# Optimization experiments

Hardware: AMD Instinct MI355X
Metric: run time of the kernel (lower is better)

## Reference

```python
import jax, jax.numpy as jnp
import numpy as np

B, T, D, H = 2, 2048, 1024, 16
DK = D // H


def setup_inputs() -> dict:
    key = jax.random.key(0)
    ks = jax.random.split(key, 11)
    s = 1.0 / np.sqrt(D)
    return {
        "x_q": jax.random.normal(ks[0], (B, T, D), jnp.float32),
        "x_kv": jax.random.normal(ks[1], (B, T, D), jnp.float32),
        "mask": jnp.ones((B, 1, T, T), jnp.int32),
        "Wq": jax.random.normal(ks[2], (D, D), jnp.float32) * s,
        "bq": jnp.zeros((D,), jnp.float32),
        "Wk": jax.random.normal(ks[3], (D, D), jnp.float32) * s,
        "bk": jnp.zeros((D,), jnp.float32),
        "Wv": jax.random.normal(ks[4], (D, D), jnp.float32) * s,
        "bv": jnp.zeros((D,), jnp.float32),
        "Wo": jax.random.normal(ks[5], (D, D), jnp.float32) * s,
        "bo": jnp.zeros((D,), jnp.float32),
    }


def _split_heads(x):
    # (B, T, D) -> (B, H, T, DK)
    b, t, _ = x.shape
    return x.reshape(b, t, H, DK).transpose(0, 2, 1, 3)


def reference(x_q, x_kv, mask, Wq, bq, Wk, bk, Wv, bv, Wo, bo):
    # Linear layers use torch convention: y = x @ W.T + b
    Q = _split_heads(x_q @ Wq.T + bq)   # (B,H,Tq,DK)
    K = _split_heads(x_kv @ Wk.T + bk)  # (B,H,Tk,DK)
    V = _split_heads(x_kv @ Wv.T + bv)  # (B,H,Tk,DK)

    scores = jnp.einsum("bhqd,bhkd->bhqk", Q, K) / jnp.sqrt(jnp.float32(DK))
    scores = jnp.where(mask == 0, jnp.float32(-jnp.inf), scores)
    attn = jax.nn.softmax(scores, axis=-1)  # (B,H,Tq,Tk)

    out = jnp.einsum("bhqk,bhkd->bhqd", attn, V)
    out = out.transpose(0, 2, 1, 3).reshape(B, T, D)  # combine heads
    out = out @ Wo.T + bo
    return out, attn
```

## Files before the change

kernel.cpp:

```cpp
#include <hip/hip_runtime.h>
#include <hip/hip_bf16.h>

#define DEVINL __device__ __forceinline__

typedef __attribute__((ext_vector_type(4))) float f32x4;
typedef __attribute__((ext_vector_type(8))) short short8;
typedef __attribute__((ext_vector_type(4))) short short4v;

constexpr int CB = 2, CT = 2048, CD = 1024, CH = 16, CDK = 64;
constexpr int CM = CB * CT;
constexpr float LOG2E = 1.44269504088896340736f;

DEVINL ushort f2bf(float f) {
  __hip_bfloat16 h = __float2bfloat16(f);
  ushort u; __builtin_memcpy(&u, &h, 2); return u;
}

DEVINL float bf2f(ushort u) {
  uint x = ((uint)u) << 16; float f; __builtin_memcpy(&f, &x, 4); return f;
}

DEVINL void gl2lds16(const ushort* g, ushort* ldsbase) {
  __builtin_amdgcn_global_load_lds(
      (const __attribute__((address_space(1))) void*)g,
      (__attribute__((address_space(3))) void*)ldsbase, 16, 0, 0);
}

__global__ void prep_kernel(const float* __restrict__ s0, ushort* __restrict__ d0, int n0,
                            const float* __restrict__ s1, ushort* __restrict__ d1, int n1,
                            const float* __restrict__ s2, ushort* __restrict__ d2, int n2,
                            const float* __restrict__ s3, ushort* __restrict__ d3, int n3,
                            const float* __restrict__ s4, ushort* __restrict__ d4, int n4,
                            const float* __restrict__ s5, ushort* __restrict__ d5, int n5,
                            const int* __restrict__ mask, uint* __restrict__ flags,
                            int cvt_blocks)
{
  if ((int)blockIdx.x >= cvt_blocks) {
    const int tile = blockIdx.x - cvt_blocks;
    const int b = tile >> 10, qb = (tile >> 5) & 31, kb = tile & 31;
    const int* base = mask + ((size_t)b * CT + qb * 64) * CT + kb * 64;
    const int r = threadIdx.x >> 2, c0 = (threadIdx.x & 3) * 16;
    int ok = 1;
    for (int j = 0; j < 4; ++j) {
      int4 v = *reinterpret_cast<const int4*>(base + (size_t)r * CT + c0 + j * 4);
      ok &= (v.x != 0) & (v.y != 0) & (v.z != 0) & (v.w != 0);
    }
    __shared__ int red[4];
    unsigned long long bal = __ballot(ok);
    if ((threadIdx.x & 63) == 0) red[threadIdx.x >> 6] = (bal == ~0ull);
    __syncthreads();
    if (threadIdx.x == 0) flags[tile] = (uint)(red[0] & red[1] & red[2] & red[3]);
    return;
  }
  int i = (blockIdx.x * blockDim.x + threadIdx.x) * 4;
  const float* s; ushort* d;
  if (i < n0) { s = s0; d = d0; }
  else if ((i -= n0) < n1) { s = s1; d = d1; }
  else if ((i -= n1) < n2) { s = s2; d = d2; }
  else if ((i -= n2) < n3) { s = s3; d = d3; }
  else if ((i -= n3) < n4) { s = s4; d = d4; }
  else if ((i -= n4) < n5) { s = s5; d = d5; }
  else return;
  float4 v = *reinterpret_cast<const float4*>(s + i);
  ushort4 o;
  o.x = f2bf(v.x); o.y = f2bf(v.y); o.z = f2bf(v.z); o.w = f2bf(v.w);
  *reinterpret_cast<ushort4*>(d + i) = o;
}

__global__ __launch_bounds__(256, 2)
void gemm_nt_kernel(const ushort* __restrict__ A, const ushort* __restrict__ Bm,
                    const float* __restrict__ bias1, const float* __restrict__ bias2,
                    void* __restrict__ Out, void* __restrict__ Out2,
                    int M, int N, int K, int mode, float scale)
{
  constexpr int BM = 128, BN = 64, BK = 32;
  __shared__ __align__(16) ushort As[2][BM * BK];
  __shared__ __align__(16) ushort Bs[2][BN * BK];
  const int tid = threadIdx.x;
  const int lane = tid & 63, wid = tid >> 6;
  const int wr = wid >> 1, wc = wid & 1;
  const int bm0 = blockIdx.y * BM, bn0 = blockIdx.x * BN;
  const int rsel = lane & 15, ksel = (lane >> 4) * 8;
  const int srow = lane >> 2, sc8 = (lane & 3) * 8;

  f32x4 acc[4][2];
  for (int i = 0; i < 4; ++i) for (int j = 0; j < 2; ++j) acc[i][j] = f32x4{0.f, 0.f, 0.f, 0.f};

  auto stage = [&](int bu, int k0) {
    const int ra0 = wid * 32;
    gl2lds16(&A[(size_t)(bm0 + ra0 + srow) * K + k0 + sc8],      &As[bu][ra0 * BK]);
    gl2lds16(&A[(size_t)(bm0 + ra0 + 16 + srow) * K + k0 + sc8], &As[bu][(ra0 + 16) * BK]);
    const int rb0 = wid * 16;
    gl2lds16(&Bm[(size_t)(bn0 + rb0 + srow) * K + k0 + sc8],     &Bs[bu][rb0 * BK]);
  };

  stage(0, 0);
  __syncthreads();
  const int NKT = K / BK;
  int bu = 0;
  for (int kt = 0; kt < NKT; ++kt) {
    if (kt + 1 < NKT) stage(bu ^ 1, (kt + 1) * BK);
    short8 af[4], bfr[2];
    for (int mi = 0; mi < 4; ++mi)
      af[mi] = *reinterpret_cast<short8*>(&As[bu][(wr * 64 + mi * 16 + rsel) * BK + ksel]);
    for (int ni = 0; ni < 2; ++ni)
      bfr[ni] = *reinterpret_cast<short8*>(&Bs[bu][(wc * 32 + ni * 16 + rsel) * BK + ksel]);
    for (int mi = 0; mi < 4; ++mi)
      for (int ni = 0; ni < 2; ++ni)
        acc[mi][ni] = __builtin_amdgcn_mfma_f32_16x16x32_bf16(af[mi], bfr[ni], acc[mi][ni], 0, 0, 0);
    if (kt + 1 < NKT) { __syncthreads(); bu ^= 1; }
  }

  const int r0 = (lane >> 4) * 4;
  for (int mi = 0; mi < 4; ++mi)
    for (int ni = 0; ni < 2; ++ni) {
      int gj = bn0 + wc * 32 + ni * 16 + rsel;
      float bv = (mode == 3 && gj >= 1024) ? bias2[gj - 1024] : bias1[gj];
      for (int r = 0; r < 4; ++r) {
        int gi = bm0 + wr * 64 + mi * 16 + r0 + r;
        float v = (acc[mi][ni][r] + bv) * scale;
        if (mode == 2) {
          reinterpret_cast<float*>(Out)[(size_t)gi * N + gj] = v;
        } else {
          int bb = gi >> 11, t = gi & (CT - 1);
          if (mode == 3 && gj >= 1024) {
            int gjv = gj - 1024;
            reinterpret_cast<ushort*>(Out2)[(((size_t)(bb * CH + (gjv >> 6)) * CDK + (gjv & 63)) * CT + t)] = f2bf(v);
          } else {
            reinterpret_cast<ushort*>(Out)[(((size_t)(bb * CH + (gj >> 6)) * CT + t) * CDK + (gj & 63))] = f2bf(v);
          }
        }
      }
    }
}

__global__ __launch_bounds__(512, 6)
void attn_kernel(const ushort* __restrict__ Qb, const ushort* __restrict__ Kb,
                 const ushort* __restrict__ Vt, const int* __restrict__ mask,
                 const uint* __restrict__ flags,
                 float* __restrict__ attn_out, ushort* __restrict__ oh)
{
  __shared__ __align__(16) ushort Ks[2][64 * 64];
  __shared__ __align__(16) ushort Vs[2][64 * 64];
  __shared__ __align__(16) ushort Pf[8][16 * 64];

  const int tid = threadIdx.x, wid = tid >> 6, lane = tid & 63;
  const int bh = blockIdx.y, b = bh >> 4, h = bh & 15;
  const int q0 = blockIdx.x * 128 + wid * 16;
  const int rsel = lane & 15, grp = lane >> 4, ksel = grp * 8;
  const int swz = rsel & 7;
  const uint* fl = flags + (b << 10) + ((q0 >> 6) << 5);
  const ushort* kpan = Kb + (size_t)bh * CT * CDK;
  const ushort* vpan = Vt + (size_t)bh * CDK * CT;

  const int strow = tid >> 3, stc = (tid & 7) ^ (strow & 7);

  auto stageK = [&](int bu, int k0) {
    gl2lds16(&kpan[(size_t)(k0 + strow) * CDK + stc * 8], &Ks[bu][(size_t)wid * 512]);
  };
  auto stageV = [&](int bu, int k0) {
    gl2lds16(&vpan[(size_t)strow * CT + k0 + stc * 8], &Vs[bu][(size_t)wid * 512]);
  };

  short8 qa0, qa1;
  {
    const ushort* qrow = Qb + ((size_t)bh * CT + q0 + rsel) * CDK;
    qa0 = *reinterpret_cast<const short8*>(qrow + ksel);
    qa1 = *reinterpret_cast<const short8*>(qrow + 32 + ksel);
  }

  const int* mrow = mask + (size_t)b * CT * CT;
  const int qme = q0 + rsel;

  float l_lane = 0.f;
  stageK(0, 0);
  __syncthreads();
  int bu = 0;
  for (int kt = 0; kt < 32; ++kt) {
    const int k0 = kt * 64;
    if (kt + 1 < 32) stageK(bu ^ 1, k0 + 64);
    const uint f = fl[kt];
    for (int ni = 0; ni < 4; ++ni) {
      const int krow = ni * 16 + rsel;
      short8 kb0 = *reinterpret_cast<short8*>(&Ks[bu][krow * 64 + ((grp    ) ^ swz) * 8]);
      short8 kb1 = *reinterpret_cast<short8*>(&Ks[bu][krow * 64 + ((grp + 4) ^ swz) * 8]);
      f32x4 z = {0.f, 0.f, 0.f, 0.f};
      z = __builtin_amdgcn_mfma_f32_16x16x32_bf16(kb0, qa0, z, 0, 0, 0);
      z = __builtin_amdgcn_mfma_f32_16x16x32_bf16(kb1, qa1, z, 0, 0, 0);
      if (f) {
        l_lane += exp2f(z[0]) + exp2f(z[1]) + exp2f(z[2]) + exp2f(z[3]);
      } else {
        const int kb_ = k0 + ni * 16 + grp * 4;
        for (int r = 0; r < 4; ++r)
          l_lane += mrow[(size_t)qme * CT + kb_ + r] ? exp2f(z[r]) : 0.f;
      }
    }
    __syncthreads();
    bu ^= 1;
  }
  l_lane += __shfl_xor(l_lane, 16, 64);
  l_lane += __shfl_xor(l_lane, 32, 64);
  const float ll = __log2f(l_lane);

  f32x4 oacc[4];
  for (int nd = 0; nd < 4; ++nd) oacc[nd] = f32x4{0.f, 0.f, 0.f, 0.f};
  float* apan = attn_out + (size_t)bh * CT * CT;
  ushort* pw = &Pf[wid][0];

  stageK(0, 0);
  stageV(0, 0);
  asm volatile("s_waitcnt vmcnt(0)" ::: "memory");
  __builtin_amdgcn_s_barrier();
  asm volatile("" ::: "memory");
  bu = 0;
  for (int kt = 0; kt < 32; ++kt) {
    const int k0 = kt * 64;
    if (kt + 1 < 32) { stageK(bu ^ 1, k0 + 64); stageV(bu ^ 1, k0 + 64); }
    asm volatile("" ::: "memory");
    const uint f = fl[kt];
    for (int ni = 0; ni < 4; ++ni) {
      const int krow = ni * 16 + rsel;
      short8 kb0 = *reinterpret_cast<short8*>(&Ks[bu][krow * 64 + ((grp    ) ^ swz) * 8]);
      short8 kb1 = *reinterpret_cast<short8*>(&Ks[bu][krow * 64 + ((grp + 4) ^ swz) * 8]);
      f32x4 z = {0.f, 0.f, 0.f, 0.f};
      z = __builtin_amdgcn_mfma_f32_16x16x32_bf16(kb0, qa0, z, 0, 0, 0);
      z = __builtin_amdgcn_mfma_f32_16x16x32_bf16(kb1, qa1, z, 0, 0, 0);
      float p0, p1, p2, p3;
      if (f) {
        p0 = exp2f(z[0] - ll); p1 = exp2f(z[1] - ll);
        p2 = exp2f(z[2] - ll); p3 = exp2f(z[3] - ll);
      } else {
        const size_t mb = (size_t)qme * CT + k0 + ni * 16 + grp * 4;
        p0 = mrow[mb + 0] ? exp2f(z[0] - ll) : 0.f;
        p1 = mrow[mb + 1] ? exp2f(z[1] - ll) : 0.f;
        p2 = mrow[mb + 2] ? exp2f(z[2] - ll) : 0.f;
        p3 = mrow[mb + 3] ? exp2f(z[3] - ll) : 0.f;
      }
      const int chpos = (2 * ni + (grp >> 1)) ^ swz;
      short4v pk = {(short)f2bf(p0), (short)f2bf(p1), (short)f2bf(p2), (short)f2bf(p3)};
      *reinterpret_cast<short4v*>(&pw[rsel * 64 + chpos * 8 + (grp & 1) * 4]) = pk;
    }
    for (int rr = 0; rr < 4; ++rr) {
      const int row = rr * 4 + grp;
      const int rs = row & 7;
      short4v pv4 = *reinterpret_cast<short4v*>(
          &pw[row * 64 + (((rsel >> 1) ^ rs)) * 8 + (rsel & 1) * 4]);
      f32x4 v = {bf2f((ushort)pv4[0]), bf2f((ushort)pv4[1]),
                 bf2f((ushort)pv4[2]), bf2f((ushort)pv4[3])};
      __builtin_nontemporal_store(v,
          reinterpret_cast<f32x4*>(apan + (size_t)(q0 + row) * CT + k0 + rsel * 4));
    }
    short8 pa0 = *reinterpret_cast<short8*>(&pw[rsel * 64 + ((grp    ) ^ swz) * 8]);
    short8 pa1 = *reinterpret_cast<short8*>(&pw[rsel * 64 + ((grp + 4) ^ swz) * 8]);
    for (int nd = 0; nd < 4; ++nd) {
      const int vrow = nd * 16 + rsel;
      short8 vb0 = *reinterpret_cast<short8*>(&Vs[bu][vrow * 64 + ((grp    ) ^ swz) * 8]);
      short8 vb1 = *reinterpret_cast<short8*>(&Vs[bu][vrow * 64 + ((grp + 4) ^ swz) * 8]);
      oacc[nd] = __builtin_amdgcn_mfma_f32_16x16x32_bf16(pa0, vb0, oacc[nd], 0, 0, 0);
      oacc[nd] = __builtin_amdgcn_mfma_f32_16x16x32_bf16(pa1, vb1, oacc[nd], 0, 0, 0);
    }
    asm volatile("s_waitcnt vmcnt(4)" ::: "memory");
    __builtin_amdgcn_s_barrier();
    asm volatile("" ::: "memory");
    bu ^= 1;
  }

  for (int nd = 0; nd < 4; ++nd)
    for (int r = 0; r < 4; ++r) {
      int q = q0 + grp * 4 + r, d = nd * 16 + rsel;
      oh[((size_t)b * CT + q) * CD + h * CDK + d] = f2bf(oacc[nd][r]);
    }
}

extern "C" void kernel_launch(void* const* d_in, const int* in_sizes, int n_in,
                              void* d_out, int out_size, void* d_ws, size_t ws_size,
                              hipStream_t stream)
{
  const float* x_q  = (const float*)d_in[0];
  const float* x_kv = (const float*)d_in[1];
  const int*   mask = (const int*)d_in[2];
  const float* Wq = (const float*)d_in[3];
  const float* bq = (const float*)d_in[4];
  const float* Wk = (const float*)d_in[5];
  const float* bk = (const float*)d_in[6];
  const float* Wv = (const float*)d_in[7];
  const float* bv = (const float*)d_in[8];
  const float* Wo = (const float*)d_in[9];
  const float* bo = (const float*)d_in[10];

  float* out  = (float*)d_out;
  float* attn = out + (size_t)CB * CT * CD;

  char* w = (char*)d_ws;
  auto alloc = [&](size_t bytes) { char* p = w; w += (bytes + 255) & ~(size_t)255; return p; };
  ushort* xq_bf  = (ushort*)alloc((size_t)CM * CD * 2);
  ushort* xkv_bf = (ushort*)alloc((size_t)CM * CD * 2);
  ushort* Wq_bf  = (ushort*)alloc((size_t)CD * CD * 2);
  ushort* Wk_bf  = (ushort*)alloc((size_t)CD * CD * 2);
  ushort* Wv_bf  = (ushort*)alloc((size_t)CD * CD * 2);
  ushort* Wo_bf  = (ushort*)alloc((size_t)CD * CD * 2);
  ushort* Q_bf   = (ushort*)alloc((size_t)CM * CD * 2);
  ushort* K_bf   = (ushort*)alloc((size_t)CM * CD * 2);
  ushort* Vt_bf  = (ushort*)alloc((size_t)CM * CD * 2);
  ushort* oh_bf  = (ushort*)alloc((size_t)CM * CD * 2);
  uint*   mflags = (uint*)alloc(2048 * sizeof(uint));

  {
    const int nx = CM * CD, nw = CD * CD;
    const int cvt_blocks = ((2 * nx + 4 * nw) / 4 + 255) / 256;
    hipLaunchKernelGGL(prep_kernel, dim3(cvt_blocks + 2048), dim3(256), 0, stream,
                       x_q, xq_bf, nx, x_kv, xkv_bf, nx,
                       Wq, Wq_bf, nw, Wk, Wk_bf, nw,
                       Wv, Wv_bf, nw, Wo, Wo_bf, nw,
                       mask, mflags, cvt_blocks);
  }

  hipLaunchKernelGGL(gemm_nt_kernel, dim3(CD / 64, CM / 128), dim3(256), 0, stream,
                     xq_bf, Wq_bf, bq, bq, (void*)Q_bf, nullptr, CM, CD, CD, 0, 0.125f * LOG2E);
  hipLaunchKernelGGL(gemm_nt_kernel, dim3(2 * CD / 64, CM / 128), dim3(256), 0, stream,
                     xkv_bf, Wk_bf, bk, bv, (void*)K_bf, (void*)Vt_bf, CM, 2 * CD, CD, 3, 1.0f);

  hipLaunchKernelGGL(attn_kernel, dim3(CT / 128, CB * CH), dim3(512), 0, stream,
                     Q_bf, K_bf, Vt_bf, mask, mflags, attn, oh_bf);

  hipLaunchKernelGGL(gemm_nt_kernel, dim3(CD / 64, CM / 128), dim3(256), 0, stream,
                     oh_bf, Wo_bf, bo, bo, d_out, nullptr, CM, CD, CD, 2, 1.0f);
}
```

Measured before the change: 285.8 us.

## Fuse row-sum pass of second query tile into first tile's output pass

Each attention block now handles two 128-row query tiles. The softmax-denominator pass for tile B is computed inside tile A's probability/PV pass, so the K tiles already staged there are reused. This cuts the number of K-streaming passes from four to three per pair of tiles. In exchange the grid is halved to 256 blocks, launch bounds drop to 2 blocks per SM, and register pressure rises, which may reduce occupancy and parallelism.

```diff
diff --git a/kernel.cpp b/kernel.cpp
--- a/kernel.cpp
+++ b/kernel.cpp
@@ -134,7 +134,7 @@
     }
 }
 
-__global__ __launch_bounds__(512, 6)
+__global__ __launch_bounds__(512, 2)
 void attn_kernel(const ushort* __restrict__ Qb, const ushort* __restrict__ Kb,
                  const ushort* __restrict__ Vt, const int* __restrict__ mask,
                  const uint* __restrict__ flags,
@@ -146,10 +146,12 @@
 
   const int tid = threadIdx.x, wid = tid >> 6, lane = tid & 63;
   const int bh = blockIdx.y, b = bh >> 4, h = bh & 15;
-  const int q0 = blockIdx.x * 128 + wid * 16;
+  const int q0A = blockIdx.x * 256 + wid * 16;
+  const int q0B = q0A + 128;
   const int rsel = lane & 15, grp = lane >> 4, ksel = grp * 8;
   const int swz = rsel & 7;
-  const uint* fl = flags + (b << 10) + ((q0 >> 6) << 5);
+  const uint* flA = flags + (b << 10) + ((q0A >> 6) << 5);
+  const uint* flB = flags + (b << 10) + ((q0B >> 6) << 5);
   const ushort* kpan = Kb + (size_t)bh * CT * CDK;
   const ushort* vpan = Vt + (size_t)bh * CDK * CT;
 
@@ -162,50 +164,54 @@
     gl2lds16(&vpan[(size_t)strow * CT + k0 + stc * 8], &Vs[bu][(size_t)wid * 512]);
   };
 
-  short8 qa0, qa1;
+  short8 qaA0, qaA1, qaB0, qaB1;
   {
-    const ushort* qrow = Qb + ((size_t)bh * CT + q0 + rsel) * CDK;
-    qa0 = *reinterpret_cast<const short8*>(qrow + ksel);
-    qa1 = *reinterpret_cast<const short8*>(qrow + 32 + ksel);
+    const ushort* qrowA = Qb + ((size_t)bh * CT + q0A + rsel) * CDK;
+    qaA0 = *reinterpret_cast<const short8*>(qrowA + ksel);
+    qaA1 = *reinterpret_cast<const short8*>(qrowA + 32 + ksel);
+    const ushort* qrowB = Qb + ((size_t)bh * CT + q0B + rsel) * CDK;
+    qaB0 = *reinterpret_cast<const short8*>(qrowB + ksel);
+    qaB1 = *reinterpret_cast<const short8*>(qrowB + 32 + ksel);
   }
 
   const int* mrow = mask + (size_t)b * CT * CT;
-  const int qme = q0 + rsel;
-
-  float l_lane = 0.f;
+  const int qmeA = q0A + rsel, qmeB = q0B + rsel;
+  float* apan = attn_out + (size_t)bh * CT * CT;
+  ushort* pw = &Pf[wid][0];
+
+  float lA = 0.f;
   stageK(0, 0);
   __syncthreads();
   int bu = 0;
   for (int kt = 0; kt < 32; ++kt) {
     const int k0 = kt * 64;
     if (kt + 1 < 32) stageK(bu ^ 1, k0 + 64);
-    const uint f = fl[kt];
+    const uint f = flA[kt];
     for (int ni = 0; ni < 4; ++ni) {
       const int krow = ni * 16 + rsel;
       short8 kb0 = *reinterpret_cast<short8*>(&Ks[bu][krow * 64 + ((grp    ) ^ swz) * 8]);
       short8 kb1 = *reinterpret_cast<short8*>(&Ks[bu][krow * 64 + ((grp + 4) ^ swz) * 8]);
       f32x4 z = {0.f, 0.f, 0.f, 0.f};
-      z = __builtin_amdgcn_mfma_f32_16x16x32_bf16(kb0, qa0, z, 0, 0, 0);
-      z = __builtin_amdgcn_mfma_f32_16x16x32_bf16(kb1, qa1, z, 0, 0, 0);
+      z = __builtin_amdgcn_mfma_f32_16x16x32_bf16(kb0, qaA0, z, 0, 0, 0);
+      z = __builtin_amdgcn_mfma_f32_16x16x32_bf16(kb1, qaA1, z, 0, 0, 0);
       if (f) {
-        l_lane += exp2f(z[0]) + exp2f(z[1]) + exp2f(z[2]) + exp2f(z[3]);
+        lA += exp2f(z[0]) + exp2f(z[1]) + exp2f(z[2]) + exp2f(z[3]);
       } else {
         const int kb_ = k0 + ni * 16 + grp * 4;
         for (int r = 0; r < 4; ++r)
-          l_lane += mrow[(size_t)qme * CT + kb_ + r] ? exp2f(z[r]) : 0.f;
+          lA += mrow[(size_t)qmeA * CT + kb_ + r] ? exp2f(z[r]) : 0.f;
       }
     }
     __syncthreads();
     bu ^= 1;
   }
-  l_lane += __shfl_xor(l_lane, 16, 64);
-  l_lane += __shfl_xor(l_lane, 32, 64);
-  const float ll = __log2f(l_lane);
+  lA += __shfl_xor(lA, 16, 64);
+  lA += __shfl_xor(lA, 32, 64);
+  const float llA = __log2f(lA);
 
   f32x4 oacc[4];
   for (int nd = 0; nd < 4; ++nd) oacc[nd] = f32x4{0.f, 0.f, 0.f, 0.f};
-  float* apan = attn_out + (size_t)bh * CT * CT;
-  ushort* pw = &Pf[wid][0];
+  float lB = 0.f;
 
   stageK(0, 0);
   stageV(0, 0);
@@ -217,24 +223,36 @@
     const int k0 = kt * 64;
     if (kt + 1 < 32) { stageK(bu ^ 1, k0 + 64); stageV(bu ^ 1, k0 + 64); }
     asm volatile("" ::: "memory");
-    const uint f = fl[kt];
+    const uint fA = flA[kt], fB = flB[kt];
     for (int ni = 0; ni < 4; ++ni) {
       const int krow = ni * 16 + rsel;
       short8 kb0 = *reinterpret_cast<short8*>(&Ks[bu][krow * 64 + ((grp    ) ^ swz) * 8]);
       short8 kb1 = *reinterpret_cast<short8*>(&Ks[bu][krow * 64 + ((grp + 4) ^ swz) * 8]);
+      {
+        f32x4 z = {0.f, 0.f, 0.f, 0.f};
+        z = __builtin_amdgcn_mfma_f32_16x16x32_bf16(kb0, qaB0, z, 0, 0, 0);
+        z = __builtin_amdgcn_mfma_f32_16x16x32_bf16(kb1, qaB1, z, 0, 0, 0);
+        if (fB) {
+          lB += exp2f(z[0]) + exp2f(z[1]) + exp2f(z[2]) + exp2f(z[3]);
+        } else {
+          const int kb_ = k0 + ni * 16 + grp * 4;
+          for (int r = 0; r < 4; ++r)
+            lB += mrow[(size_t)qmeB * CT + kb_ + r] ? exp2f(z[r]) : 0.f;
+        }
+      }
       f32x4 z = {0.f, 0.f, 0.f, 0.f};
-      z = __builtin_amdgcn_mfma_f32_16x16x32_bf16(kb0, qa0, z, 0, 0, 0);
-      z = __builtin_amdgcn_mfma_f32_16x16x32_bf16(kb1, qa1, z, 0, 0, 0);
+      z = __builtin_amdgcn_mfma_f32_16x16x32_bf16(kb0, qaA0, z, 0, 0, 0);
+      z = __builtin_amdgcn_mfma_f32_16x16x32_bf16(kb1, qaA1, z, 0, 0, 0);
       float p0, p1, p2, p3;
-      if (f) {
-        p0 = exp2f(z[0] - ll); p1 = exp2f(z[1] - ll);
-        p2 = exp2f(z[2] - ll); p3 = exp2f(z[3] - ll);
+      if (fA) {
+        p0 = exp2f(z[0] - llA); p1 = exp2f(z[1] - llA);
+        p2 = exp2f(z[2] - llA); p3 = exp2f(z[3] - llA);
       } else {
-        const size_t mb = (size_t)qme * CT + k0 + ni * 16 + grp * 4;
-        p0 = mrow[mb + 0] ? exp2f(z[0] - ll) : 0.f;
-        p1 = mrow[mb + 1] ? exp2f(z[1] - ll) : 0.f;
-        p2 = mrow[mb + 2] ? exp2f(z[2] - ll) : 0.f;
-        p3 = mrow[mb + 3] ? exp2f(z[3] - ll) : 0.f;
+        const size_t mb = (size_t)qmeA * CT + k0 + ni * 16 + grp * 4;
+        p0 = mrow[mb + 0] ? exp2f(z[0] - llA) : 0.f;
+        p1 = mrow[mb + 1] ? exp2f(z[1] - llA) : 0.f;
+        p2 = mrow[mb + 2] ? exp2f(z[2] - llA) : 0.f;
+        p3 = mrow[mb + 3] ? exp2f(z[3] - llA) : 0.f;
       }
       const int chpos = (2 * ni + (grp >> 1)) ^ swz;
       short4v pk = {(short)f2bf(p0), (short)f2bf(p1), (short)f2bf(p2), (short)f2bf(p3)};
@@ -248,7 +266,7 @@
       f32x4 v = {bf2f((ushort)pv4[0]), bf2f((ushort)pv4[1]),
                  bf2f((ushort)pv4[2]), bf2f((ushort)pv4[3])};
       __builtin_nontemporal_store(v,
-          reinterpret_cast<f32x4*>(apan + (size_t)(q0 + row) * CT + k0 + rsel * 4));
+          reinterpret_cast<f32x4*>(apan + (size_t)(q0A + row) * CT + k0 + rsel * 4));
     }
     short8 pa0 = *reinterpret_cast<short8*>(&pw[rsel * 64 + ((grp    ) ^ swz) * 8]);
     short8 pa1 = *reinterpret_cast<short8*>(&pw[rsel * 64 + ((grp + 4) ^ swz) * 8]);
@@ -264,10 +282,76 @@
     asm volatile("" ::: "memory");
     bu ^= 1;
   }
-
   for (int nd = 0; nd < 4; ++nd)
     for (int r = 0; r < 4; ++r) {
-      int q = q0 + grp * 4 + r, d = nd * 16 + rsel;
+      int q = q0A + grp * 4 + r, d = nd * 16 + rsel;
+      oh[((size_t)b * CT + q) * CD + h * CDK + d] = f2bf(oacc[nd][r]);
+    }
+  lB += __shfl_xor(lB, 16, 64);
+  lB += __shfl_xor(lB, 32, 64);
+  const float llB = __log2f(lB);
+
+  for (int nd = 0; nd < 4; ++nd) oacc[nd] = f32x4{0.f, 0.f, 0.f, 0.f};
+  stageK(0, 0);
+  stageV(0, 0);
+  asm volatile("s_waitcnt vmcnt(0)" ::: "memory");
+  __builtin_amdgcn_s_barrier();
+  asm volatile("" ::: "memory");
+  bu = 0;
+  for (int kt = 0; kt < 32; ++kt) {
+    const int k0 = kt * 64;
+    if (kt + 1 < 32) { stageK(bu ^ 1, k0 + 64); stageV(bu ^ 1, k0 + 64); }
+    asm volatile("" ::: "memory");
+    const uint f = flB[kt];
+    for (int ni = 0; ni < 4; ++ni) {
+      const int krow = ni * 16 + rsel;
+      short8 kb0 = *reinterpret_cast<short8*>(&Ks[bu][krow * 64 + ((grp    ) ^ swz) * 8]);
+      short8 kb1 = *reinterpret_cast<short8*>(&Ks[bu][krow * 64 + ((grp + 4) ^ swz) * 8]);
+      f32x4 z = {0.f, 0.f, 0.f, 0.f};
+      z = __builtin_amdgcn_mfma_f32_16x16x32_bf16(kb0, qaB0, z, 0, 0, 0);
+      z = __builtin_amdgcn_mfma_f32_16x16x32_bf16(kb1, qaB1, z, 0, 0, 0);
+      float p0, p1, p2, p3;
+      if (f) {
+        p0 = exp2f(z[0] - llB); p1 = exp2f(z[1] - llB);
+        p2 = exp2f(z[2] - llB); p3 = exp2f(z[3] - llB);
+      } else {
+        const size_t mb = (size_t)qmeB * CT + k0 + ni * 16 + grp * 4;
+        p0 = mrow[mb + 0] ? exp2f(z[0] - llB) : 0.f;
+        p1 = mrow[mb + 1] ? exp2f(z[1] - llB) : 0.f;
+        p2 = mrow[mb + 2] ? exp2f(z[2] - llB) : 0.f;
+        p3 = mrow[mb + 3] ? exp2f(z[3] - llB) : 0.f;
+      }
+      const int chpos = (2 * ni + (grp >> 1)) ^ swz;
+      short4v pk = {(short)f2bf(p0), (short)f2bf(p1), (short)f2bf(p2), (short)f2bf(p3)};
+      *reinterpret_cast<short4v*>(&pw[rsel * 64 + chpos * 8 + (grp & 1) * 4]) = pk;
+    }
+    for (int rr = 0; rr < 4; ++rr) {
+      const int row = rr * 4 + grp;
+      const int rs = row & 7;
+      short4v pv4 = *reinterpret_cast<short4v*>(
+          &pw[row * 64 + (((rsel >> 1) ^ rs)) * 8 + (rsel & 1) * 4]);
+      f32x4 v = {bf2f((ushort)pv4[0]), bf2f((ushort)pv4[1]),
+                 bf2f((ushort)pv4[2]), bf2f((ushort)pv4[3])};
+      __builtin_nontemporal_store(v,
+          reinterpret_cast<f32x4*>(apan + (size_t)(q0B + row) * CT + k0 + rsel * 4));
+    }
+    short8 pa0 = *reinterpret_cast<short8*>(&pw[rsel * 64 + ((grp    ) ^ swz) * 8]);
+    short8 pa1 = *reinterpret_cast<short8*>(&pw[rsel * 64 + ((grp + 4) ^ swz) * 8]);
+    for (int nd = 0; nd < 4; ++nd) {
+      const int vrow = nd * 16 + rsel;
+      short8 vb0 = *reinterpret_cast<short8*>(&Vs[bu][vrow * 64 + ((grp    ) ^ swz) * 8]);
+      short8 vb1 = *reinterpret_cast<short8*>(&Vs[bu][vrow * 64 + ((grp + 4) ^ swz) * 8]);
+      oacc[nd] = __builtin_amdgcn_mfma_f32_16x16x32_bf16(pa0, vb0, oacc[nd], 0, 0, 0);
+      oacc[nd] = __builtin_amdgcn_mfma_f32_16x16x32_bf16(pa1, vb1, oacc[nd], 0, 0, 0);
+    }
+    asm volatile("s_waitcnt vmcnt(4)" ::: "memory");
+    __builtin_amdgcn_s_barrier();
+    asm volatile("" ::: "memory");
+    bu ^= 1;
+  }
+  for (int nd = 0; nd < 4; ++nd)
+    for (int r = 0; r < 4; ++r) {
+      int q = q0B + grp * 4 + r, d = nd * 16 + rsel;
       oh[((size_t)b * CT + q) * CD + h * CDK + d] = f2bf(oacc[nd][r]);
     }
 }
@@ -320,7 +404,7 @@
   hipLaunchKernelGGL(gemm_nt_kernel, dim3(2 * CD / 64, CM / 128), dim3(256), 0, stream,
                      xkv_bf, Wk_bf, bk, bv, (void*)K_bf, (void*)Vt_bf, CM, 2 * CD, CD, 3, 1.0f);
 
-  hipLaunchKernelGGL(attn_kernel, dim3(CT / 128, CB * CH), dim3(512), 0, stream,
+  hipLaunchKernelGGL(attn_kernel, dim3(CT / 256, CB * CH), dim3(512), 0, stream,
                      Q_bf, K_bf, Vt_bf, mask, mflags, attn, oh_bf);
 
   hipLaunchKernelGGL(gemm_nt_kernel, dim3(CD / 64, CM / 128), dim3(256), 0, stream,
```

Result: no change. 281.7 us (median of 2 runs) (-1.4%).
